# Kernel tuning notes

Measured on AMD Instinct MI355X. Metric: run time of the kernel, lower is better.

## Reference

```python
import jax, jax.numpy as jnp
import numpy as np

DIM = 512        # model dim
MOE_DIM = 256    # expert hidden dim
E = 64           # n_routed experts
G = 8            # n_routed_group
TOPK_G = 4       # n_topk_group
K = 8            # n_experts_per_tok
SCALE = 2.5      # routed_scale
CAP = 1024


def setup_inputs() -> dict:
    key = jax.random.key(0)
    ks = jax.random.split(key, 6)
    x = jax.random.normal(ks[0], (4, 512, DIM), jnp.float32)
    gate_w = jax.random.normal(ks[1], (E, DIM), jnp.float32) / np.sqrt(DIM).astype(np.float32)
    gate_b = jax.random.normal(ks[2], (E,), jnp.float32) * 0.01
    w1 = jax.random.normal(ks[3], (E, DIM, MOE_DIM), jnp.float32) / np.sqrt(DIM).astype(np.float32)
    w3 = jax.random.normal(ks[4], (E, DIM, MOE_DIM), jnp.float32) / np.sqrt(DIM).astype(np.float32)
    w2 = jax.random.normal(ks[5], (E, MOE_DIM, DIM), jnp.float32) / np.sqrt(MOE_DIM).astype(np.float32)
    return {"x": x, "gate_w": gate_w, "gate_b": gate_b, "w1": w1, "w3": w3, "w2": w2}


def _gate(x2, gate_w, gate_b):
    # x2: [T, DIM] -> (weights [T,K], indices [T,K])
    T = x2.shape[0]
    scores = jax.nn.sigmoid(x2 @ gate_w.T)                      # [T, E]
    s = (scores + gate_b).reshape(T, G, E // G)                  # grouped scores
    group_scores = jax.lax.top_k(s, 2)[0].sum(-1)                # [T, G] sum of top-2 per group
    top_groups = jax.lax.top_k(group_scores, TOPK_G)[1]          # [T, TOPK_G]
    gmask = jnp.zeros((T, G), bool).at[jnp.arange(T)[:, None], top_groups].set(True)
    s = jnp.where(gmask[..., None], s, -jnp.inf).reshape(T, E)
    idx = jax.lax.top_k(s, K)[1]                                 # [T, K]
    w = jnp.take_along_axis(scores, idx, axis=1)                 # original (pre-bias) scores
    w = w / w.sum(-1, keepdims=True) * SCALE
    return w, idx


def _moe_forward(x, gate_w, gate_b, w1, w3, w2):
    shape = x.shape
    x2 = x.reshape(-1, DIM)                                      # [T, DIM]
    T = x2.shape[0]
    w, idx = _gate(x2, gate_w, gate_b)
    flat_e = idx.reshape(-1)                                     # [T*K]
    # position of each (token, slot) within its expert's buffer, in order
    oh = (flat_e[:, None] == jnp.arange(E)[None, :]).astype(jnp.int32)  # [T*K, E]
    pos = (jnp.cumsum(oh, axis=0) * oh).sum(-1) - 1              # [T*K]
    x_rep = jnp.repeat(x2, K, axis=0)                            # [T*K, DIM]
    # dispatch into per-expert buffers [E, CAP, DIM]
    xb = jnp.zeros((E, CAP, DIM), x2.dtype).at[flat_e, pos].set(x_rep, mode='drop')
    h = jax.nn.silu(jnp.einsum('ecd,edm->ecm', xb, w1)) * jnp.einsum('ecd,edm->ecm', xb, w3)
    yb = jnp.einsum('ecm,emd->ecd', h, w2)                       # [E, CAP, DIM]
    # combine: gather back and weight
    y = yb.at[flat_e, pos].get(mode='fill', fill_value=0.0) * w.reshape(-1)[:, None]
    return y.reshape(T, K, DIM).sum(1).reshape(shape)


def reference(x, gate_w, gate_b, w1, w3, w2):
    return _moe_forward(x, gate_w, gate_b, w1, w3, w2)
```

## Files before the change

kernel.cpp:

```cpp
#include <hip/hip_runtime.h>

#define T_TOK 2048
#define DIM   512
#define MOE   256
#define NE    64
#define NG    8
#define TOPKG 4
#define TOPK  8
#define CAP   1024
#define MOE_SCALE 2.5f

typedef float f32x4 __attribute__((ext_vector_type(4)));
typedef short s16x8 __attribute__((ext_vector_type(8)));

__device__ __forceinline__ unsigned short f2bf(float f) {
    unsigned u = __builtin_bit_cast(unsigned, f);
    unsigned r = (u + 0x7fffu + ((u >> 16) & 1u)) >> 16;
    return (unsigned short)r;
}
__device__ __forceinline__ unsigned pk2(float lo, float hi) {
    return (unsigned)f2bf(lo) | ((unsigned)f2bf(hi) << 16);
}

__global__ __launch_bounds__(256) void gwt_k(const float* __restrict__ gw,
                                             float* __restrict__ gwT)
{
    int idx = blockIdx.x * 256 + threadIdx.x;
    int e = idx >> 9, k = idx & 511;
    gwT[(size_t)(k >> 2) * 256 + e * 4 + (k & 3)] = gw[idx];
}

__global__ __launch_bounds__(256) void gate_fused_k(const float* __restrict__ x,
                                                    const float* __restrict__ gwT,
                                                    const float* __restrict__ gb,
                                                    int* __restrict__ counts,
                                                    int* __restrict__ etok,
                                                    float* __restrict__ wt_of,
                                                    short* __restrict__ xb)
{
    __shared__ float xs[4][512];
    int w = threadIdx.x >> 6, lane = threadIdx.x & 63;
    int t = blockIdx.x * 4 + w;

    {
        const float4* xr = (const float4*)(x + (size_t)t * DIM);
        float4 v0 = xr[lane * 2], v1 = xr[lane * 2 + 1];
        *(float4*)&xs[w][lane * 8]     = v0;
        *(float4*)&xs[w][lane * 8 + 4] = v1;
        short o[8];
        o[0] = (short)f2bf(v0.x); o[1] = (short)f2bf(v0.y);
        o[2] = (short)f2bf(v0.z); o[3] = (short)f2bf(v0.w);
        o[4] = (short)f2bf(v1.x); o[5] = (short)f2bf(v1.y);
        o[6] = (short)f2bf(v1.z); o[7] = (short)f2bf(v1.w);
        *(s16x8*)(xb + (size_t)t * DIM + lane * 8) = *(const s16x8*)o;
    }
    __syncthreads();

    const float4* gt = (const float4*)gwT;
    float a0 = 0.f, a1 = 0.f, a2 = 0.f, a3 = 0.f;
#pragma unroll 4
    for (int k4 = 0; k4 < 128; k4 += 4) {
        float4 g0 = gt[(k4 + 0) * 64 + lane];
        float4 g1 = gt[(k4 + 1) * 64 + lane];
        float4 g2 = gt[(k4 + 2) * 64 + lane];
        float4 g3 = gt[(k4 + 3) * 64 + lane];
        float4 x0 = *(const float4*)&xs[w][(k4 + 0) * 4];
        float4 x1 = *(const float4*)&xs[w][(k4 + 1) * 4];
        float4 x2 = *(const float4*)&xs[w][(k4 + 2) * 4];
        float4 x3 = *(const float4*)&xs[w][(k4 + 3) * 4];
        a0 += g0.x * x0.x + g0.y * x0.y + g0.z * x0.z + g0.w * x0.w;
        a1 += g1.x * x1.x + g1.y * x1.y + g1.z * x1.z + g1.w * x1.w;
        a2 += g2.x * x2.x + g2.y * x2.y + g2.z * x2.z + g2.w * x2.w;
        a3 += g3.x * x3.x + g3.y * x3.y + g3.z * x3.z + g3.w * x3.w;
    }
    float acc = (a0 + a1) + (a2 + a3);
    float sc = 1.f / (1.f + __expf(-acc));
    float s  = sc + gb[lane];

    float m1 = s, m2 = -1e30f;
#pragma unroll
    for (int d = 1; d < 8; d <<= 1) {
        float o1 = __shfl_xor(m1, d);
        float o2 = __shfl_xor(m2, d);
        float n1 = fmaxf(m1, o1);
        float n2 = fmaxf(fminf(m1, o1), fmaxf(m2, o2));
        m1 = n1; m2 = n2;
    }
    float gv = m1 + m2;

    bool gkeep = false;
#pragma unroll
    for (int it = 0; it < TOPKG; ++it) {
        float m = gv;
#pragma unroll
        for (int d = 1; d < 64; d <<= 1) m = fmaxf(m, __shfl_xor(m, d));
        unsigned long long mask = __ballot(gv == m);
        int ldr = __ffsll(mask) - 1;
        if ((lane >> 3) == (ldr >> 3)) { gkeep = true; gv = -2e30f; }
    }
    float sv = gkeep ? s : -1e30f;

    float wsum = 0.f;
    int my_e = 0; float my_w = 0.f;
#pragma unroll
    for (int k = 0; k < TOPK; ++k) {
        float m = sv;
#pragma unroll
        for (int d = 1; d < 64; d <<= 1) m = fmaxf(m, __shfl_xor(m, d));
        unsigned long long mask = __ballot(sv == m);
        int l = __ffsll(mask) - 1;
        float wk = __shfl(sc, l);
        wsum += wk;
        if (lane == k) { my_e = l; my_w = wk; }
        if (lane == l) sv = -2e30f;
    }
    float scale = MOE_SCALE / wsum;
    if (lane < TOPK) {
        int p = atomicAdd(&counts[my_e], 1);
        int rid = t * TOPK + lane;
        bool ok = (p < CAP);
        if (ok) etok[my_e * CAP + p] = rid;
        wt_of[rid] = ok ? my_w * scale : 0.f;
    }
}

__global__ __launch_bounds__(256) void gemm1_k(const short* __restrict__ xb,
                                               const float* __restrict__ w1,
                                               const float* __restrict__ w3,
                                               const int* __restrict__ counts,
                                               const int* __restrict__ etok,
                                               short* __restrict__ hbuf)
{
    __shared__ short Bl[2][2][16][64][8];

    int e  = blockIdx.x >> 3, cg = blockIdx.x & 7;
    int n0 = cg * 32;
    int tid = threadIdx.x;
    int w = tid >> 6, lane = tid & 63;
    int q = lane >> 4, m16 = lane & 15;

    const float* W1e = w1 + (size_t)e * DIM * MOE + n0;
    const float* W3e = w3 + (size_t)e * DIM * MOE + n0;
#pragma unroll
    for (int it = 0; it < 8; ++it) {
        int idx = it * 256 + tid;
        int r2  = idx >> 3;
        int cq  = (idx & 7) * 4;
        int k   = r2 * 2;
        int kt = k >> 5, qq = (k >> 3) & 3, j0 = k & 7;
        int s = cq >> 4, c15 = cq & 15;
        const float* p1 = W1e + (size_t)k * MOE + cq;
        const float* p3 = W3e + (size_t)k * MOE + cq;
        float4 lo1 = *(const float4*)p1;
        float4 hi1 = *(const float4*)(p1 + MOE);
        float4 lo3 = *(const float4*)p3;
        float4 hi3 = *(const float4*)(p3 + MOE);
        unsigned* b0 = (unsigned*)&Bl[0][s][kt][qq * 16 + c15][j0];
        b0[0]  = pk2(lo1.x, hi1.x);
        b0[4]  = pk2(lo1.y, hi1.y);
        b0[8]  = pk2(lo1.z, hi1.z);
        b0[12] = pk2(lo1.w, hi1.w);
        unsigned* b1 = (unsigned*)&Bl[1][s][kt][qq * 16 + c15][j0];
        b1[0]  = pk2(lo3.x, hi3.x);
        b1[4]  = pk2(lo3.y, hi3.y);
        b1[8]  = pk2(lo3.z, hi3.z);
        b1[12] = pk2(lo3.w, hi3.w);
    }
    __syncthreads();

    int n_e = min(counts[e], CAP);
    int ntiles = (n_e + 31) >> 5;
    const int* el = etok + e * CAP;

    for (int tile = w; tile < ntiles; tile += 4) {
        int r0 = tile * 32;
        int row0 = r0 + m16, row1 = r0 + 16 + m16;
        int tok0 = el[row0 < n_e ? row0 : n_e - 1] >> 3;
        int tok1 = el[row1 < n_e ? row1 : n_e - 1] >> 3;
        const short* A0 = xb + (size_t)tok0 * DIM + q * 8;
        const short* A1 = xb + (size_t)tok1 * DIM + q * 8;

        f32x4 g0[2], g1[2], u0[2], u1[2];
#pragma unroll
        for (int s = 0; s < 2; ++s) {
            g0[s] = (f32x4)0.f; g1[s] = (f32x4)0.f;
            u0[s] = (f32x4)0.f; u1[s] = (f32x4)0.f;
        }
#pragma unroll
        for (int kt = 0; kt < 16; ++kt) {
            s16x8 a0 = *(const s16x8*)(A0 + kt * 32);
            s16x8 a1 = *(const s16x8*)(A1 + kt * 32);
#pragma unroll
            for (int s = 0; s < 2; ++s) {
                s16x8 b1 = *(const s16x8*)&Bl[0][s][kt][lane][0];
                g0[s] = __builtin_amdgcn_mfma_f32_16x16x32_bf16(a0, b1, g0[s], 0, 0, 0);
                g1[s] = __builtin_amdgcn_mfma_f32_16x16x32_bf16(a1, b1, g1[s], 0, 0, 0);
                s16x8 b3 = *(const s16x8*)&Bl[1][s][kt][lane][0];
                u0[s] = __builtin_amdgcn_mfma_f32_16x16x32_bf16(a0, b3, u0[s], 0, 0, 0);
                u1[s] = __builtin_amdgcn_mfma_f32_16x16x32_bf16(a1, b3, u1[s], 0, 0, 0);
            }
        }
#pragma unroll
        for (int s = 0; s < 2; ++s) {
#pragma unroll
            for (int r = 0; r < 4; ++r) {
                int rr0 = r0 + q * 4 + r;
                if (rr0 < n_e) {
                    float g = g0[s][r], uu = u0[s][r];
                    float hv = g / (1.f + __expf(-g)) * uu;
                    hbuf[(size_t)el[rr0] * MOE + n0 + s * 16 + m16] = (short)f2bf(hv);
                }
                int rr1 = r0 + 16 + q * 4 + r;
                if (rr1 < n_e) {
                    float g = g1[s][r], uu = u1[s][r];
                    float hv = g / (1.f + __expf(-g)) * uu;
                    hbuf[(size_t)el[rr1] * MOE + n0 + s * 16 + m16] = (short)f2bf(hv);
                }
            }
        }
    }
}

__global__ __launch_bounds__(256) void gemm2_k(const short* __restrict__ hbuf,
                                               const float* __restrict__ w2,
                                               const int* __restrict__ counts,
                                               const int* __restrict__ etok,
                                               short* __restrict__ ybuf)
{
    __shared__ short Bl[4][8][64][8];

    int e  = blockIdx.x >> 3, cg = blockIdx.x & 7;
    int n0 = cg * 64;
    int tid = threadIdx.x;
    int w = tid >> 6, lane = tid & 63;
    int q = lane >> 4, m16 = lane & 15;

    const float* W2e = w2 + (size_t)e * MOE * DIM + n0;
#pragma unroll
    for (int it = 0; it < 8; ++it) {
        int idx = it * 256 + tid;
        int r2  = idx >> 4;
        int cq  = (idx & 15) * 4;
        int k   = r2 * 2;
        int kt = k >> 5, qq = (k >> 3) & 3, j0 = k & 7;
        int s = cq >> 4, c15 = cq & 15;
        const float* p2 = W2e + (size_t)k * DIM + cq;
        float4 lo = *(const float4*)p2;
        float4 hi = *(const float4*)(p2 + DIM);
        unsigned* b = (unsigned*)&Bl[s][kt][qq * 16 + c15][j0];
        b[0]  = pk2(lo.x, hi.x);
        b[4]  = pk2(lo.y, hi.y);
        b[8]  = pk2(lo.z, hi.z);
        b[12] = pk2(lo.w, hi.w);
    }
    __syncthreads();

    int n_e = min(counts[e], CAP);
    int ntiles = (n_e + 31) >> 5;
    const int* el = etok + e * CAP;

    for (int tile = w; tile < ntiles; tile += 4) {
        int r0 = tile * 32;
        int row0 = r0 + m16, row1 = r0 + 16 + m16;
        int rid0 = el[row0 < n_e ? row0 : n_e - 1];
        int rid1 = el[row1 < n_e ? row1 : n_e - 1];
        const short* A0 = hbuf + (size_t)rid0 * MOE + q * 8;
        const short* A1 = hbuf + (size_t)rid1 * MOE + q * 8;

        f32x4 y0[4], y1[4];
#pragma unroll
        for (int s = 0; s < 4; ++s) { y0[s] = (f32x4)0.f; y1[s] = (f32x4)0.f; }
#pragma unroll
        for (int kt = 0; kt < 8; ++kt) {
            s16x8 a0 = *(const s16x8*)(A0 + kt * 32);
            s16x8 a1 = *(const s16x8*)(A1 + kt * 32);
#pragma unroll
            for (int s = 0; s < 4; ++s) {
                s16x8 b = *(const s16x8*)&Bl[s][kt][lane][0];
                y0[s] = __builtin_amdgcn_mfma_f32_16x16x32_bf16(a0, b, y0[s], 0, 0, 0);
                y1[s] = __builtin_amdgcn_mfma_f32_16x16x32_bf16(a1, b, y1[s], 0, 0, 0);
            }
        }
#pragma unroll
        for (int s = 0; s < 4; ++s) {
#pragma unroll
            for (int r = 0; r < 4; ++r) {
                int rr0 = r0 + q * 4 + r;
                if (rr0 < n_e)
                    ybuf[(size_t)el[rr0] * DIM + n0 + s * 16 + m16] = (short)f2bf(y0[s][r]);
                int rr1 = r0 + 16 + q * 4 + r;
                if (rr1 < n_e)
                    ybuf[(size_t)el[rr1] * DIM + n0 + s * 16 + m16] = (short)f2bf(y1[s][r]);
            }
        }
    }
}

__global__ __launch_bounds__(256) void combine_k(const short* __restrict__ ybuf,
                                                 const float* __restrict__ wt_of,
                                                 float* __restrict__ out)
{
    int t = blockIdx.x;
    int tid = threadIdx.x;
    const int* yb = (const int*)ybuf;
    float sx = 0.f, sy = 0.f;
#pragma unroll
    for (int k = 0; k < TOPK; ++k) {
        float wk = wt_of[t * TOPK + k];
        int v = yb[(size_t)(t * TOPK + k) * (DIM / 2) + tid];
        float lo = __builtin_bit_cast(float, (unsigned)v << 16);
        float hi = __builtin_bit_cast(float, (unsigned)v & 0xffff0000u);
        sx += wk * lo;
        sy += wk * hi;
    }
    float2 o = {sx, sy};
    ((float2*)out)[(size_t)t * (DIM / 2) + tid] = o;
}

extern "C" void kernel_launch(void* const* d_in, const int* in_sizes, int n_in,
                              void* d_out, int out_size, void* d_ws, size_t ws_size,
                              hipStream_t stream)
{
    const float* x  = (const float*)d_in[0];
    const float* gw = (const float*)d_in[1];
    const float* gb = (const float*)d_in[2];
    const float* w1 = (const float*)d_in[3];
    const float* w3 = (const float*)d_in[4];
    const float* w2 = (const float*)d_in[5];

    char* ws = (char*)d_ws;
    short* xb    = (short*)(ws);
    short* hbuf  = (short*)(ws + 2097152);
    short* ybuf  = (short*)(ws + 10485760);
    float* gwT   = (float*)(ws + 27262976);
    int*   etok  = (int*)  (ws + 27394048);
    float* wt_of = (float*)(ws + 27656192);
    int*   counts= (int*)  (ws + 27721728);

    hipMemsetAsync(counts, 0, NE * 4, stream);

    gwt_k<<<128, 256, 0, stream>>>(gw, gwT);
    gate_fused_k<<<T_TOK / 4, 256, 0, stream>>>(x, gwT, gb, counts, etok, wt_of, xb);
    gemm1_k<<<NE * 8, 256, 0, stream>>>(xb, w1, w3, counts, etok, hbuf);
    gemm2_k<<<NE * 8, 256, 0, stream>>>(hbuf, w2, counts, etok, ybuf);
    combine_k<<<T_TOK, 256, 0, stream>>>(ybuf, wt_of, (float*)d_out);
}
```

Before: 266.0 us.

## Pre-gather expert tokens into MFMA-fragment layout and stream contiguous tiles

Adds a scan kernel that computes per-expert tile offsets and a gather kernel that copies each expert's token rows into a packed, fragment-ordered buffer, so the two GEMM kernels read their A operands contiguously instead of through scattered token indirection. gemm1 now stages its SwiGLU output through shared memory and writes it in the same fragment layout that gemm2 consumes directly. The block index mapping is also swapped so that consecutive blocks cover different experts. In exchange there are two extra kernel launches and an extra pass that writes and rereads the gathered activations.

Result: slower. 277.0 us (+4.2%).

```diff
diff --git a/kernel.cpp b/kernel.cpp
--- a/kernel.cpp
+++ b/kernel.cpp
@@ -124,16 +124,63 @@
     }
 }
 
-__global__ __launch_bounds__(256) void gemm1_k(const short* __restrict__ xb,
+__global__ __launch_bounds__(64) void scan_k(const int* __restrict__ counts,
+                                             int* __restrict__ tbase)
+{
+    int lane = threadIdx.x;
+    int ne = min(counts[lane], CAP);
+    int nt = (ne + 31) >> 5;
+    int v = nt;
+#pragma unroll
+    for (int d = 1; d < 64; d <<= 1) {
+        int o = __shfl_up(v, d);
+        if (lane >= d) v += o;
+    }
+    tbase[lane] = v - nt;
+}
+
+__global__ __launch_bounds__(256) void gather_k(const short* __restrict__ xb,
+                                                const int* __restrict__ counts,
+                                                const int* __restrict__ etok,
+                                                const int* __restrict__ tbase,
+                                                short* __restrict__ xgf)
+{
+    int e = blockIdx.x >> 3, sub3 = blockIdx.x & 7;
+    int w = threadIdx.x >> 6, lane = threadIdx.x & 63;
+    int T = sub3 * 4 + w;
+    int ne = min(counts[e], CAP);
+    int nt = (ne + 31) >> 5;
+    if (T >= nt) return;
+    int G = tbase[e] + T;
+    int q = lane >> 4, m16 = lane & 15;
+    int r0 = T * 32 + m16, r1 = T * 32 + 16 + m16;
+    bool ok0 = r0 < ne, ok1 = r1 < ne;
+    int tok0 = ok0 ? (etok[e * CAP + r0] >> 3) : 0;
+    int tok1 = ok1 ? (etok[e * CAP + r1] >> 3) : 0;
+    const short* s0 = xb + (size_t)tok0 * DIM + q * 8;
+    const short* s1 = xb + (size_t)tok1 * DIM + q * 8;
+    short* dst = xgf + (size_t)G * 32 * 512 + lane * 8;
+    s16x8 z = {0, 0, 0, 0, 0, 0, 0, 0};
+#pragma unroll
+    for (int kt = 0; kt < 16; ++kt) {
+        s16x8 a0 = ok0 ? *(const s16x8*)(s0 + kt * 32) : z;
+        s16x8 a1 = ok1 ? *(const s16x8*)(s1 + kt * 32) : z;
+        *(s16x8*)(dst + (size_t)(kt * 2 + 0) * 512) = a0;
+        *(s16x8*)(dst + (size_t)(kt * 2 + 1) * 512) = a1;
+    }
+}
+
+__global__ __launch_bounds__(256) void gemm1_k(const short* __restrict__ xgf,
                                                const float* __restrict__ w1,
                                                const float* __restrict__ w3,
                                                const int* __restrict__ counts,
-                                               const int* __restrict__ etok,
-                                               short* __restrict__ hbuf)
+                                               const int* __restrict__ tbase,
+                                               short* __restrict__ hgf)
 {
     __shared__ short Bl[2][2][16][64][8];
-
-    int e  = blockIdx.x >> 3, cg = blockIdx.x & 7;
+    __shared__ short Ct[4][16][34];
+
+    int e  = blockIdx.x & 63, cg = blockIdx.x >> 6;
     int n0 = cg * 32;
     int tid = threadIdx.x;
     int w = tid >> 6, lane = tid & 63;
@@ -168,17 +215,13 @@
     }
     __syncthreads();
 
-    int n_e = min(counts[e], CAP);
-    int ntiles = (n_e + 31) >> 5;
-    const int* el = etok + e * CAP;
-
-    for (int tile = w; tile < ntiles; tile += 4) {
-        int r0 = tile * 32;
-        int row0 = r0 + m16, row1 = r0 + 16 + m16;
-        int tok0 = el[row0 < n_e ? row0 : n_e - 1] >> 3;
-        int tok1 = el[row1 < n_e ? row1 : n_e - 1] >> 3;
-        const short* A0 = xb + (size_t)tok0 * DIM + q * 8;
-        const short* A1 = xb + (size_t)tok1 * DIM + q * 8;
+    int ne = min(counts[e], CAP);
+    int nt = (ne + 31) >> 5;
+    int G0 = tbase[e];
+    short* ct = &Ct[w][0][0];
+
+    for (int T = w; T < nt; T += 4) {
+        const short* A = xgf + (size_t)(G0 + T) * 32 * 512 + lane * 8;
 
         f32x4 g0[2], g1[2], u0[2], u1[2];
 #pragma unroll
@@ -188,8 +231,8 @@
         }
 #pragma unroll
         for (int kt = 0; kt < 16; ++kt) {
-            s16x8 a0 = *(const s16x8*)(A0 + kt * 32);
-            s16x8 a1 = *(const s16x8*)(A1 + kt * 32);
+            s16x8 a0 = *(const s16x8*)(A + (size_t)(kt * 2 + 0) * 512);
+            s16x8 a1 = *(const s16x8*)(A + (size_t)(kt * 2 + 1) * 512);
 #pragma unroll
             for (int s = 0; s < 2; ++s) {
                 s16x8 b1 = *(const s16x8*)&Bl[0][s][kt][lane][0];
@@ -201,35 +244,32 @@
             }
         }
 #pragma unroll
-        for (int s = 0; s < 2; ++s) {
-#pragma unroll
-            for (int r = 0; r < 4; ++r) {
-                int rr0 = r0 + q * 4 + r;
-                if (rr0 < n_e) {
-                    float g = g0[s][r], uu = u0[s][r];
+        for (int sub = 0; sub < 2; ++sub) {
+#pragma unroll
+            for (int s = 0; s < 2; ++s)
+#pragma unroll
+                for (int r = 0; r < 4; ++r) {
+                    float g = sub ? g1[s][r] : g0[s][r];
+                    float uu = sub ? u1[s][r] : u0[s][r];
                     float hv = g / (1.f + __expf(-g)) * uu;
-                    hbuf[(size_t)el[rr0] * MOE + n0 + s * 16 + m16] = (short)f2bf(hv);
+                    ct[(q * 4 + r) * 34 + s * 16 + m16] = (short)f2bf(hv);
                 }
-                int rr1 = r0 + 16 + q * 4 + r;
-                if (rr1 < n_e) {
-                    float g = g1[s][r], uu = u1[s][r];
-                    float hv = g / (1.f + __expf(-g)) * uu;
-                    hbuf[(size_t)el[rr1] * MOE + n0 + s * 16 + m16] = (short)f2bf(hv);
-                }
-            }
+            s16x8 hv8 = *(const s16x8*)&ct[m16 * 34 + q * 8];
+            *(s16x8*)(hgf + (size_t)(((G0 + T) * 8 + cg) * 2 + sub) * 512 + lane * 8) = hv8;
         }
     }
 }
 
-__global__ __launch_bounds__(256) void gemm2_k(const short* __restrict__ hbuf,
+__global__ __launch_bounds__(256) void gemm2_k(const short* __restrict__ hgf,
                                                const float* __restrict__ w2,
                                                const int* __restrict__ counts,
                                                const int* __restrict__ etok,
+                                               const int* __restrict__ tbase,
                                                short* __restrict__ ybuf)
 {
     __shared__ short Bl[4][8][64][8];
 
-    int e  = blockIdx.x >> 3, cg = blockIdx.x & 7;
+    int e  = blockIdx.x & 63, cg = blockIdx.x >> 6;
     int n0 = cg * 64;
     int tid = threadIdx.x;
     int w = tid >> 6, lane = tid & 63;
@@ -255,25 +295,21 @@
     }
     __syncthreads();
 
-    int n_e = min(counts[e], CAP);
-    int ntiles = (n_e + 31) >> 5;
+    int ne = min(counts[e], CAP);
+    int nt = (ne + 31) >> 5;
+    int G0 = tbase[e];
     const int* el = etok + e * CAP;
 
-    for (int tile = w; tile < ntiles; tile += 4) {
-        int r0 = tile * 32;
-        int row0 = r0 + m16, row1 = r0 + 16 + m16;
-        int rid0 = el[row0 < n_e ? row0 : n_e - 1];
-        int rid1 = el[row1 < n_e ? row1 : n_e - 1];
-        const short* A0 = hbuf + (size_t)rid0 * MOE + q * 8;
-        const short* A1 = hbuf + (size_t)rid1 * MOE + q * 8;
+    for (int T = w; T < nt; T += 4) {
+        const short* A = hgf + (size_t)(G0 + T) * 16 * 512 + lane * 8;
 
         f32x4 y0[4], y1[4];
 #pragma unroll
         for (int s = 0; s < 4; ++s) { y0[s] = (f32x4)0.f; y1[s] = (f32x4)0.f; }
 #pragma unroll
         for (int kt = 0; kt < 8; ++kt) {
-            s16x8 a0 = *(const s16x8*)(A0 + kt * 32);
-            s16x8 a1 = *(const s16x8*)(A1 + kt * 32);
+            s16x8 a0 = *(const s16x8*)(A + (size_t)(kt * 2 + 0) * 512);
+            s16x8 a1 = *(const s16x8*)(A + (size_t)(kt * 2 + 1) * 512);
 #pragma unroll
             for (int s = 0; s < 4; ++s) {
                 s16x8 b = *(const s16x8*)&Bl[s][kt][lane][0];
@@ -282,17 +318,16 @@
             }
         }
 #pragma unroll
-        for (int s = 0; s < 4; ++s) {
+        for (int s = 0; s < 4; ++s)
 #pragma unroll
             for (int r = 0; r < 4; ++r) {
-                int rr0 = r0 + q * 4 + r;
-                if (rr0 < n_e)
-                    ybuf[(size_t)el[rr0] * DIM + n0 + s * 16 + m16] = (short)f2bf(y0[s][r]);
-                int rr1 = r0 + 16 + q * 4 + r;
-                if (rr1 < n_e)
-                    ybuf[(size_t)el[rr1] * DIM + n0 + s * 16 + m16] = (short)f2bf(y1[s][r]);
+                int row0 = T * 32 + q * 4 + r;
+                if (row0 < ne)
+                    ybuf[(size_t)el[row0] * DIM + n0 + s * 16 + m16] = (short)f2bf(y0[s][r]);
+                int row1 = row0 + 16;
+                if (row1 < ne)
+                    ybuf[(size_t)el[row1] * DIM + n0 + s * 16 + m16] = (short)f2bf(y1[s][r]);
             }
-        }
     }
 }
 
@@ -330,18 +365,22 @@
 
     char* ws = (char*)d_ws;
     short* xb    = (short*)(ws);
-    short* hbuf  = (short*)(ws + 2097152);
-    short* ybuf  = (short*)(ws + 10485760);
-    float* gwT   = (float*)(ws + 27262976);
-    int*   etok  = (int*)  (ws + 27394048);
-    float* wt_of = (float*)(ws + 27656192);
-    int*   counts= (int*)  (ws + 27721728);
+    short* xgf   = (short*)(ws + 2097152);
+    short* hgf   = (short*)(ws + 20971520);
+    short* ybuf  = (short*)(ws + 30408704);
+    float* gwT   = (float*)(ws + 47185920);
+    int*   etok  = (int*)  (ws + 47316992);
+    float* wt_of = (float*)(ws + 47579136);
+    int*   counts= (int*)  (ws + 47644672);
+    int*   tbase = (int*)  (ws + 47644928);
 
     hipMemsetAsync(counts, 0, NE * 4, stream);
 
     gwt_k<<<128, 256, 0, stream>>>(gw, gwT);
     gate_fused_k<<<T_TOK / 4, 256, 0, stream>>>(x, gwT, gb, counts, etok, wt_of, xb);
-    gemm1_k<<<NE * 8, 256, 0, stream>>>(xb, w1, w3, counts, etok, hbuf);
-    gemm2_k<<<NE * 8, 256, 0, stream>>>(hbuf, w2, counts, etok, ybuf);
+    scan_k<<<1, 64, 0, stream>>>(counts, tbase);
+    gather_k<<<NE * 8, 256, 0, stream>>>(xb, counts, etok, tbase, xgf);
+    gemm1_k<<<NE * 8, 256, 0, stream>>>(xgf, w1, w3, counts, tbase, hgf);
+    gemm2_k<<<NE * 8, 256, 0, stream>>>(hgf, w2, counts, etok, tbase, ybuf);
     combine_k<<<T_TOK, 256, 0, stream>>>(ybuf, wt_of, (float*)d_out);
 }
```
